# Kernel tuning notes

Hardware: AMD Instinct MI355X
Metric: run time of the kernel (lower is better)

The kernel has to match this reference:

```python
import jax, jax.numpy as jnp
import numpy as np

EPS = 1e-8

def _penalty(v, lo, hi):
    # if v<lo: (lo-v)/lo ; elif v>hi (hi finite): (v-hi)/hi ; else 0
    below = (lo - v) / lo
    if np.isinf(hi):
        return jnp.where(v < lo, below, 0.0)
    above = (v - hi) / hi
    return jnp.where(v < lo, below, jnp.where(v > hi, above, 0.0))

def _symbolic_features(x):
    # x: [B, input_dim]; column mapping from the original per-row loop
    am, bod, do, ph, nit = x[:, 0], x[:, 1], x[:, 2], x[:, 4], x[:, 7]
    # penalties in param_order = [ph, ammonia, bod, dissolved_oxygen, nitrate]
    p_ph  = _penalty(ph, 6.5, 8.5)
    p_am  = _penalty(am, 0.001, 0.5)
    p_bod = _penalty(bod, 0.001, 5.0)
    p_do  = _penalty(do, 6.0, np.inf)
    p_nit = _penalty(nit, 0.001, 10.0)
    # pollutant scores (missing params like 'nitrogen'/'orthophosphate' are skipped -> count adjusts)
    s_bact = (1.2 * am / (0.5 + EPS) + 1.5 * bod / (5.0 + EPS) - 0.8 * do / (10.0 + EPS)) / 3.0
    s_chem = (1.5 * ph / (8.5 + EPS) + 1.0 * nit / (10.0 + EPS)) / 2.0
    s_org  = (2.0 * bod / (5.0 + EPS) - 1.5 * do / (10.0 + EPS) + 0.8 * am / (0.5 + EPS)) / 3.0
    s_agr  = (2.0 * nit / (10.0 + EPS)) / 1.0
    resil = 1.0 / (1.0 + (p_ph + p_am + p_bod + p_do + p_nit) + EPS)
    return jnp.stack([p_ph, p_am, p_bod, p_do, p_nit, s_bact, s_chem, s_org, s_agr, resil], axis=1)

def setup_inputs() -> dict:
    key = jax.random.key(0)
    ks = jax.random.split(key, 16)
    B, D_IN, SYM, H = 1048576, 10, 10, 64
    def lin(k, fin, fout):
        k1, k2 = jax.random.split(k)
        s = 1.0 / np.sqrt(fin)
        return (jax.random.uniform(k1, (fin, fout), jnp.float32, -s, s),
                jax.random.uniform(k2, (fout,), jnp.float32, -s, s))
    W_sym, b_sym = lin(ks[0], SYM, H // 2)
    W_in, b_in = lin(ks[1], D_IN + H // 2, H)
    W1, b1 = lin(ks[2], H, H)
    W2, b2 = lin(ks[3], H, H)
    W3, b3 = lin(ks[4], H, H)
    W_r1, b_r1 = lin(ks[5], H, H // 2)
    W_r2, b_r2 = lin(ks[6], H // 2, 1)
    W_c1, b_c1 = lin(ks[7], H, H // 2)
    W_c2, b_c2 = lin(ks[8], H // 2, 4)
    x = jax.random.uniform(ks[9], (B, D_IN), jnp.float32)
    return {"x": x, "W_sym": W_sym, "b_sym": b_sym, "W_in": W_in, "b_in": b_in,
            "W1": W1, "b1": b1, "W2": W2, "b2": b2, "W3": W3, "b3": b3,
            "W_r1": W_r1, "b_r1": b_r1, "W_r2": W_r2, "b_r2": b_r2,
            "W_c1": W_c1, "b_c1": b_c1, "W_c2": W_c2, "b_c2": b_c2}

def reference(x, W_sym, b_sym, W_in, b_in, W1, b1, W2, b2, W3, b3,
              W_r1, b_r1, W_r2, b_r2, W_c1, b_c1, W_c2, b_c2):
    elu = jax.nn.elu
    sym = _symbolic_features(x)                      # [B, 10]
    sym_enc = elu(sym @ W_sym + b_sym)               # [B, 32]  (Dropout: eval mode = identity)
    h = elu(jnp.concatenate([x, sym_enc], axis=1) @ W_in + b_in)  # [B, 64]
    for W, b in ((W1, b1), (W2, b2), (W3, b3)):
        h = h + elu(h @ W + b)                       # residual MLP stack
    predictions = elu(h @ W_r1 + b_r1) @ W_r2 + b_r2            # [B, 1]
    pollutant_logits = elu(h @ W_c1 + b_c1) @ W_c2 + b_c2       # [B, 4]
    return predictions, pollutant_logits
```

## Files before the change

kernel.cpp:

```cpp
#include <hip/hip_runtime.h>
#include <hip/hip_bf16.h>
#include <math.h>

#define NROWS 1048576
#define EPSF 1e-8f
#define GRID 512
#define TPB 256
#define ITERS 16

typedef unsigned short ushortT;
typedef __attribute__((ext_vector_type(8))) short short8;
typedef __attribute__((ext_vector_type(4))) short short4v;
typedef __attribute__((ext_vector_type(4))) float floatx4;
typedef __attribute__((ext_vector_type(2))) int int2v;

#define WS_HI   256
#define WS_LO   41216
#define WS_MF   82176
#define MF_B5   0
#define MF_WSYM 320
#define MF_BSYM 640
#define MF_WR2  672
#define MF_BR2  704
#define MF_WC2  708
#define MF_BC2  836
#define MF_WC2T 840
#define MF_TOTAL 968

#define LDS_FENCE() asm volatile("s_waitcnt lgkmcnt(0)" ::: "memory")

struct WPtrs { const void* p[19]; };

__global__ void sniff_kernel(const ushortT* __restrict__ x, int* __restrict__ flag) {
    if (threadIdx.x == 0 && blockIdx.x == 0) {
        unsigned s = 0;
        for (int i = 0; i < 64; ++i) s |= (unsigned)(x[i] & 0x8000u);
        *flag = s ? 1 : 0;
    }
}

__device__ __forceinline__ float ldw(const void* p, int i, bool f32) {
    return f32 ? ((const float*)p)[i]
               : __uint_as_float(((unsigned)((const ushortT*)p)[i]) << 16);
}

__global__ void prep_kernel(WPtrs wp, const int* __restrict__ flag, void* __restrict__ ws) {
    const bool f32 = (*flag != 0);
    ushortT* hi = (ushortT*)((char*)ws + WS_HI);
    ushortT* lo = (ushortT*)((char*)ws + WS_LO);
    float* mf = (float*)((char*)ws + WS_MF);
    const int B = blockIdx.x;
    if (B < 5) {
        const int L = B;
        for (int idx = threadIdx.x; idx < 4096; idx += 256) {
            const int j8 = idx & 7, ln = (idx >> 3) & 63, s2 = (idx >> 9) & 1, t = idx >> 10;
            const int s = 2 * s2 + (j8 >> 2), j = j8 & 3;
            const int k = 16 * s + 4 * (ln >> 4) + j;
            const int m = 16 * t + (ln & 15);
            float w = 0.0f;
            if (L == 0)      { if (k < 42) w = ldw(wp.p[3], k * 64 + m, f32); }
            else if (L <= 3) { if (k < 64) w = ldw(wp.p[3 + 2 * L], k * 64 + m, f32); }
            else             { if (k < 64) w = (m < 32) ? ldw(wp.p[11], k * 32 + m, f32)
                                                        : ldw(wp.p[15], k * 32 + (m - 32), f32); }
            const unsigned u = __float_as_uint(w);
            const float rem = w - __uint_as_float(u & 0xffff0000u);
            hi[L * 4096 + idx] = (ushortT)(u >> 16);
            lo[L * 4096 + idx] = (ushortT)(__float_as_uint(rem) >> 16);
        }
    } else {
        const int src[12] = {4, 6, 8, 10, 12, 16, 1, 2, 13, 14, 17, 18};
        const int cnt[12] = {64, 64, 64, 64, 32, 32, 320, 32, 32, 1, 128, 4};
        const int dst[12] = {0, 64, 128, 192, 256, 288, MF_WSYM, MF_BSYM, MF_WR2, MF_BR2, MF_WC2, MF_BC2};
        for (int a = 0; a < 12; ++a)
            for (int i = threadIdx.x; i < cnt[a]; i += 256)
                mf[dst[a] + i] = ldw(wp.p[src[a]], i, f32);
        for (int i = threadIdx.x; i < 128; i += 256) {
            const int qq = i >> 5, j = i & 31;
            mf[MF_WC2T + i] = ldw(wp.p[17], j * 4 + qq, f32);
        }
    }
}

__device__ __forceinline__ float eluf(float v) {
    return fmaxf(v, 0.0f) + (__expf(fminf(v, 0.0f)) - 1.0f);
}

__device__ __forceinline__ unsigned pack_hi16(unsigned ua, unsigned ub) {
    return __builtin_amdgcn_perm(ub, ua, 0x07060302u);
}

__device__ __forceinline__ void split4(float a0, float a1, float a2, float a3,
                                       short4v& h4, short4v& l4) {
    const unsigned u0 = __float_as_uint(a0), u1 = __float_as_uint(a1);
    const unsigned u2 = __float_as_uint(a2), u3 = __float_as_uint(a3);
    int2v h, l;
    h[0] = (int)pack_hi16(u0, u1);
    h[1] = (int)pack_hi16(u2, u3);
    const float l0 = a0 - __uint_as_float(u0 & 0xffff0000u);
    const float l1 = a1 - __uint_as_float(u1 & 0xffff0000u);
    const float l2 = a2 - __uint_as_float(u2 & 0xffff0000u);
    const float l3 = a3 - __uint_as_float(u3 & 0xffff0000u);
    l[0] = (int)pack_hi16(__float_as_uint(l0), __float_as_uint(l1));
    l[1] = (int)pack_hi16(__float_as_uint(l2), __float_as_uint(l3));
    h4 = __builtin_bit_cast(short4v, h);
    l4 = __builtin_bit_cast(short4v, l);
}

__device__ __forceinline__ floatx4 mfma16(short4v a, short4v b, floatx4 c) {
#if __has_builtin(__builtin_amdgcn_mfma_f32_16x16x16bf16_1k)
    return __builtin_amdgcn_mfma_f32_16x16x16bf16_1k(a, b, c, 0, 0, 0);
#else
    floatx4 d;
    asm("v_mfma_f32_16x16x16_bf16 %0, %1, %2, %3" : "=v"(d) : "v"(a), "v"(b), "v"(c));
    return d;
#endif
}

template<bool F32>
__device__ __forceinline__ void run_body(
    const void* __restrict__ xin, const char* __restrict__ wsb,
    void* __restrict__ out,
    const ushortT* __restrict__ wlds,
    const float* __restrict__ mflds,
    float (* __restrict__ hb)[68],
    const int lane, const int wavebase)
{
    const ushortT* __restrict__ wflo = (const ushortT*)(wsb + WS_LO);
    const int n = lane & 15, q = lane >> 4;

    #pragma unroll
    for (int i = 0; i < 6; ++i) {
        const int c = 42 + q * 6 + i;
        if (c < 64) hb[n][c] = 0.0f;
    }

    unsigned xu[2][5];
    float xf[2][10];
    #pragma unroll
    for (int u = 0; u < 2; ++u) {
        const int rowg = wavebase + 16 * u + n;
        if (F32) {
            const float* xp = (const float*)xin + (size_t)rowg * 10;
            #pragma unroll
            for (int i = 0; i < 10; ++i) xf[u][i] = xp[i];
        } else {
            const unsigned* xd = (const unsigned*)((const ushortT*)xin + (size_t)rowg * 10);
            #pragma unroll
            for (int i = 0; i < 5; ++i) xu[u][i] = xd[i];
        }
    }

    #pragma unroll 1
    for (int it = 0; it < ITERS; ++it) {
        const int rowbase = wavebase + it * 32;
        short4v Bhi[2][4], Blo[2][4];

        #pragma unroll
        for (int u = 0; u < 2; ++u) {
            float x[10];
            if (F32) {
                #pragma unroll
                for (int i = 0; i < 10; ++i) x[i] = xf[u][i];
            } else {
                #pragma unroll
                for (int i = 0; i < 5; ++i) {
                    const unsigned d = xu[u][i];
                    x[2 * i]     = __uint_as_float(d << 16);
                    x[2 * i + 1] = __uint_as_float(d & 0xffff0000u);
                }
            }
            if (q == 0) {
                #pragma unroll
                for (int i = 0; i < 10; ++i) hb[n][i] = x[i];
            }

            const float am = x[0], bod = x[1], dox = x[2], ph = x[4], nit = x[7];
            const float p_ph  = ph  < 6.5f   ? (6.5f - ph) * 0.15384616f
                              : (ph > 8.5f   ? (ph - 8.5f) * 0.11764706f : 0.0f);
            const float p_am  = am  < 0.001f ? (0.001f - am) * 1000.0f
                              : (am > 0.5f   ? (am - 0.5f) * 2.0f : 0.0f);
            const float p_bod = bod < 0.001f ? (0.001f - bod) * 1000.0f
                              : (bod > 5.0f  ? (bod - 5.0f) * 0.2f : 0.0f);
            const float p_do  = dox < 6.0f   ? (6.0f - dox) * 0.16666667f : 0.0f;
            const float p_nit = nit < 0.001f ? (0.001f - nit) * 1000.0f
                              : (nit > 10.0f ? (nit - 10.0f) * 0.1f : 0.0f);
            const float s_bact = (am * 2.3999999f + bod * 0.29999998f - dox * 0.08f) * 0.33333334f;
            const float s_chem = (ph * 0.17647059f + nit * 0.1f) * 0.5f;
            const float s_org  = (bod * 0.39999998f - dox * 0.14999999f + am * 1.5999999f) * 0.33333334f;
            const float s_agr  = nit * 0.2f;
            const float resil  = 1.0f / (1.0f + (p_ph + p_am + p_bod + p_do + p_nit) + EPSF);
            const float sym[10] = {p_ph, p_am, p_bod, p_do, p_nit, s_bact, s_chem, s_org, s_agr, resil};

            float se[8];
            {
                const floatx4 b0 = *(const floatx4*)(mflds + MF_BSYM + q * 8);
                const floatx4 b1 = *(const floatx4*)(mflds + MF_BSYM + q * 8 + 4);
                #pragma unroll
                for (int jj = 0; jj < 4; ++jj) { se[jj] = b0[jj]; se[4 + jj] = b1[jj]; }
                #pragma unroll
                for (int k = 0; k < 10; ++k) {
                    const floatx4 w0 = *(const floatx4*)(mflds + MF_WSYM + k * 32 + q * 8);
                    const floatx4 w1 = *(const floatx4*)(mflds + MF_WSYM + k * 32 + q * 8 + 4);
                    #pragma unroll
                    for (int jj = 0; jj < 4; ++jj) {
                        se[jj]     = fmaf(sym[k], w0[jj], se[jj]);
                        se[4 + jj] = fmaf(sym[k], w1[jj], se[4 + jj]);
                    }
                }
            }
            #pragma unroll
            for (int jj = 0; jj < 8; ++jj) hb[n][10 + q * 8 + jj] = eluf(se[jj]);
            LDS_FENCE();
            #pragma unroll
            for (int s = 0; s < 4; ++s) {
                const floatx4 v = *(const floatx4*)&hb[n][16 * s + 4 * q];
                split4(v[0], v[1], v[2], v[3], Bhi[u][s], Blo[u][s]);
            }
            LDS_FENCE();
        }

        {
            const int itn = (it + 1 < ITERS) ? it + 1 : it;
            #pragma unroll
            for (int u = 0; u < 2; ++u) {
                const int rowg = wavebase + itn * 32 + 16 * u + n;
                if (F32) {
                    const float* xp = (const float*)xin + (size_t)rowg * 10;
                    #pragma unroll
                    for (int i = 0; i < 10; ++i) xf[u][i] = xp[i];
                } else {
                    const unsigned* xd = (const unsigned*)((const ushortT*)xin + (size_t)rowg * 10);
                    #pragma unroll
                    for (int i = 0; i < 5; ++i) xu[u][i] = xd[i];
                }
            }
        }

        float hprev[2][4][4];
        #pragma unroll
        for (int L = 0; L < 5; ++L) {
            short8 Ap[8];
            const ushortT* wl = wlds + L * 4096 + lane * 8;
            #pragma unroll
            for (int c = 0; c < 8; ++c)
                Ap[c] = *(const short8*)(wl + c * 512);
            short8 Alp[8];
            if (F32) {
                const int base = L * 4096 + lane * 8;
                #pragma unroll
                for (int c = 0; c < 8; ++c)
                    Alp[c] = *(const short8*)(wflo + base + c * 512);
            }

            floatx4 acc[2][4];
            #pragma unroll
            for (int t = 0; t < 4; ++t) {
                const floatx4 b = *(const floatx4*)(mflds + MF_B5 + L * 64 + 16 * t + 4 * q);
                acc[0][t] = b; acc[1][t] = b;
            }
            #pragma unroll
            for (int t = 0; t < 4; ++t) {
                #pragma unroll
                for (int s2 = 0; s2 < 2; ++s2) {
                    const short8 A = Ap[t * 2 + s2];
                    const short4v ae = {A[0], A[1], A[2], A[3]};
                    const short4v ao = {A[4], A[5], A[6], A[7]};
                    #pragma unroll
                    for (int u = 0; u < 2; ++u) {
                        acc[u][t] = mfma16(ae, Bhi[u][2 * s2],     acc[u][t]);
                        acc[u][t] = mfma16(ae, Blo[u][2 * s2],     acc[u][t]);
                        acc[u][t] = mfma16(ao, Bhi[u][2 * s2 + 1], acc[u][t]);
                        acc[u][t] = mfma16(ao, Blo[u][2 * s2 + 1], acc[u][t]);
                    }
                    if (F32) {
                        const short8 Al = Alp[t * 2 + s2];
                        const short4v le  = {Al[0], Al[1], Al[2], Al[3]};
                        const short4v lo_ = {Al[4], Al[5], Al[6], Al[7]};
                        #pragma unroll
                        for (int u = 0; u < 2; ++u) {
                            acc[u][t] = mfma16(le,  Bhi[u][2 * s2],     acc[u][t]);
                            acc[u][t] = mfma16(lo_, Bhi[u][2 * s2 + 1], acc[u][t]);
                        }
                    }
                }
            }

            if (L < 4) {
                #pragma unroll
                for (int u = 0; u < 2; ++u) {
                    #pragma unroll
                    for (int t = 0; t < 4; ++t) {
                        #pragma unroll
                        for (int r = 0; r < 4; ++r) {
                            float e = eluf(acc[u][t][r]);
                            if (L >= 1) e += hprev[u][t][r];
                            hprev[u][t][r] = e;
                        }
                        split4(hprev[u][t][0], hprev[u][t][1],
                               hprev[u][t][2], hprev[u][t][3], Bhi[u][t], Blo[u][t]);
                    }
                }
            } else {
                const floatx4 wr0 = *(const floatx4*)(mflds + MF_WR2 + 4 * q);
                const floatx4 wr1 = *(const floatx4*)(mflds + MF_WR2 + 16 + 4 * q);
                #pragma unroll
                for (int u = 0; u < 2; ++u) {
                    float pred = (q == 0) ? mflds[MF_BR2] : 0.0f;
                    float z2[4], z3[4];
                    #pragma unroll
                    for (int r = 0; r < 4; ++r) {
                        pred = fmaf(eluf(acc[u][0][r]), wr0[r], pred);
                        pred = fmaf(eluf(acc[u][1][r]), wr1[r], pred);
                        z2[r] = eluf(acc[u][2][r]);
                        z3[r] = eluf(acc[u][3][r]);
                    }
                    float lg[4];
                    #pragma unroll
                    for (int c = 0; c < 4; ++c) {
                        const floatx4 wc0 = *(const floatx4*)(mflds + MF_WC2T + c * 32 + 4 * q);
                        const floatx4 wc1 = *(const floatx4*)(mflds + MF_WC2T + c * 32 + 16 + 4 * q);
                        float l = (q == 0) ? mflds[MF_BC2 + c] : 0.0f;
                        #pragma unroll
                        for (int r = 0; r < 4; ++r) {
                            l = fmaf(z2[r], wc0[r], l);
                            l = fmaf(z3[r], wc1[r], l);
                        }
                        lg[c] = l;
                    }
                    pred += __shfl_xor(pred, 16, 64);
                    pred += __shfl_xor(pred, 32, 64);
                    #pragma unroll
                    for (int c = 0; c < 4; ++c) {
                        lg[c] += __shfl_xor(lg[c], 16, 64);
                        lg[c] += __shfl_xor(lg[c], 32, 64);
                    }
                    const float lsel = q == 0 ? lg[0] : (q == 1 ? lg[1] : (q == 2 ? lg[2] : lg[3]));
                    const int rowg = rowbase + 16 * u + n;
                    if (F32) {
                        float* o = (float*)out;
                        if (q == 0) o[rowg] = pred;
                        o[NROWS + rowg * 4 + q] = lsel;
                    } else {
                        __hip_bfloat16* o = (__hip_bfloat16*)out;
                        if (q == 0) o[rowg] = __float2bfloat16(pred);
                        o[NROWS + rowg * 4 + q] = __float2bfloat16(lsel);
                    }
                }
            }
        }
    }
}

__global__ __launch_bounds__(TPB, 2) void mlp_mfma_kernel(
    const void* __restrict__ xin, const int* __restrict__ flagp,
    const void* __restrict__ ws, void* __restrict__ out)
{
    __shared__ __align__(16) ushortT wlds[5 * 4096];
    __shared__ __align__(16) float mflds[MF_TOTAL];
    __shared__ float hball[4][16][68];

    const int tid = threadIdx.x;
    {
        const unsigned* src = (const unsigned*)((const char*)ws + WS_HI);
        unsigned* dst = (unsigned*)wlds;
        for (int i = tid; i < 10240; i += TPB) dst[i] = src[i];
        const float* mfsrc = (const float*)((const char*)ws + WS_MF);
        for (int i = tid; i < MF_TOTAL; i += TPB) mflds[i] = mfsrc[i];
    }
    __syncthreads();

    const int wave = tid >> 6, lane = tid & 63;
    const int gw = blockIdx.x * 4 + wave;
    const int wavebase = gw * (32 * ITERS);
    if (*flagp != 0)
        run_body<true>(xin, (const char*)ws, out, wlds, mflds, hball[wave], lane, wavebase);
    else
        run_body<false>(xin, (const char*)ws, out, wlds, mflds, hball[wave], lane, wavebase);
}

extern "C" void kernel_launch(void* const* d_in, const int* in_sizes, int n_in,
                              void* d_out, int out_size, void* d_ws, size_t ws_size,
                              hipStream_t stream) {
    (void)in_sizes; (void)n_in; (void)out_size; (void)ws_size;
    int* flag = (int*)d_ws;

    sniff_kernel<<<1, 64, 0, stream>>>((const ushortT*)d_in[0], flag);

    WPtrs wp;
    for (int i = 0; i < 19; ++i) wp.p[i] = d_in[i];
    prep_kernel<<<6, 256, 0, stream>>>(wp, flag, d_ws);

    mlp_mfma_kernel<<<GRID, TPB, 0, stream>>>(d_in[0], flag, d_ws, d_out);
}
```

Before: 330.6 us.

## Use 16x16x32 bf16 MFMA, stream weights from global, drop sniff launch, raise occupancy

Replaces pairs of 16x16x16 bf16 MFMAs with single 16x16x32 MFMAs by packing B operands into short8. Removes the LDS copy of the weight matrices so each lane reads its A fragments straight from the workspace through cache. This frees about 40KB of LDS, which allows launch bounds of 4 blocks per SM, and the grid is doubled while iterations per wave are halved. The separate sniff kernel is dropped in favour of a ballot-based dtype check inside each kernel. The cost is more global/L2 traffic for weights on every layer, in exchange for fewer MFMA issues, one less launch, and higher occupancy.

```diff
diff --git a/kernel.cpp b/kernel.cpp
--- a/kernel.cpp
+++ b/kernel.cpp
@@ -4,9 +4,9 @@
 
 #define NROWS 1048576
 #define EPSF 1e-8f
-#define GRID 512
+#define GRID 1024
 #define TPB 256
-#define ITERS 16
+#define ITERS 8
 
 typedef unsigned short ushortT;
 typedef __attribute__((ext_vector_type(8))) short short8;
@@ -31,21 +31,26 @@
 
 struct WPtrs { const void* p[19]; };
 
-__global__ void sniff_kernel(const ushortT* __restrict__ x, int* __restrict__ flag) {
-    if (threadIdx.x == 0 && blockIdx.x == 0) {
-        unsigned s = 0;
-        for (int i = 0; i < 64; ++i) s |= (unsigned)(x[i] & 0x8000u);
-        *flag = s ? 1 : 0;
-    }
-}
-
 __device__ __forceinline__ float ldw(const void* p, int i, bool f32) {
     return f32 ? ((const float*)p)[i]
                : __uint_as_float(((unsigned)((const ushortT*)p)[i]) << 16);
 }
 
-__global__ void prep_kernel(WPtrs wp, const int* __restrict__ flag, void* __restrict__ ws) {
-    const bool f32 = (*flag != 0);
+__device__ __forceinline__ int sniff_f32(const void* x) {
+    const ushortT v = ((const ushortT*)x)[threadIdx.x & 63];
+    const unsigned long long m = __ballot((v & 0x8000u) != 0);
+    return (m != 0ull) ? 1 : 0;
+}
+
+__global__ void prep_kernel(WPtrs wp, void* __restrict__ ws) {
+    __shared__ int flagS;
+    if (threadIdx.x < 64) {
+        const int f = sniff_f32(wp.p[0]);
+        if (threadIdx.x == 0) flagS = f;
+    }
+    __syncthreads();
+    const bool f32 = (flagS != 0);
+
     ushortT* hi = (ushortT*)((char*)ws + WS_HI);
     ushortT* lo = (ushortT*)((char*)ws + WS_LO);
     float* mf = (float*)((char*)ws + WS_MF);
@@ -106,13 +111,20 @@
     l4 = __builtin_bit_cast(short4v, l);
 }
 
-__device__ __forceinline__ floatx4 mfma16(short4v a, short4v b, floatx4 c) {
-#if __has_builtin(__builtin_amdgcn_mfma_f32_16x16x16bf16_1k)
-    return __builtin_amdgcn_mfma_f32_16x16x16bf16_1k(a, b, c, 0, 0, 0);
+__device__ __forceinline__ void put4(short8& d, int hh, short4v s) {
+    d[4 * hh + 0] = s[0]; d[4 * hh + 1] = s[1];
+    d[4 * hh + 2] = s[2]; d[4 * hh + 3] = s[3];
+}
+
+__device__ __forceinline__ floatx4 mfma32(short8 a, short8 b, floatx4 c) {
+#if __has_builtin(__builtin_amdgcn_mfma_f32_16x16x32_bf16)
+    return __builtin_amdgcn_mfma_f32_16x16x32_bf16(a, b, c, 0, 0, 0);
 #else
-    floatx4 d;
-    asm("v_mfma_f32_16x16x16_bf16 %0, %1, %2, %3" : "=v"(d) : "v"(a), "v"(b), "v"(c));
-    return d;
+    const short4v ae = {a[0], a[1], a[2], a[3]}, ao = {a[4], a[5], a[6], a[7]};
+    const short4v be = {b[0], b[1], b[2], b[3]}, bo = {b[4], b[5], b[6], b[7]};
+    c = __builtin_amdgcn_mfma_f32_16x16x16bf16_1k(ae, be, c, 0, 0, 0);
+    c = __builtin_amdgcn_mfma_f32_16x16x16bf16_1k(ao, bo, c, 0, 0, 0);
+    return c;
 #endif
 }
 
@@ -120,12 +132,12 @@
 __device__ __forceinline__ void run_body(
     const void* __restrict__ xin, const char* __restrict__ wsb,
     void* __restrict__ out,
-    const ushortT* __restrict__ wlds,
     const float* __restrict__ mflds,
     float (* __restrict__ hb)[68],
     const int lane, const int wavebase)
 {
-    const ushortT* __restrict__ wflo = (const ushortT*)(wsb + WS_LO);
+    const short8* __restrict__ Ahi = (const short8*)(wsb + WS_HI) + lane;
+    const short8* __restrict__ Alo = (const short8*)(wsb + WS_LO) + lane;
     const int n = lane & 15, q = lane >> 4;
 
     #pragma unroll
@@ -153,7 +165,7 @@
     #pragma unroll 1
     for (int it = 0; it < ITERS; ++it) {
         const int rowbase = wavebase + it * 32;
-        short4v Bhi[2][4], Blo[2][4];
+        short8 Bhi8[2][2], Blo8[2][2];
 
         #pragma unroll
         for (int u = 0; u < 2; ++u) {
@@ -212,9 +224,15 @@
             for (int jj = 0; jj < 8; ++jj) hb[n][10 + q * 8 + jj] = eluf(se[jj]);
             LDS_FENCE();
             #pragma unroll
-            for (int s = 0; s < 4; ++s) {
-                const floatx4 v = *(const floatx4*)&hb[n][16 * s + 4 * q];
-                split4(v[0], v[1], v[2], v[3], Bhi[u][s], Blo[u][s]);
+            for (int s2 = 0; s2 < 2; ++s2) {
+                #pragma unroll
+                for (int hh = 0; hh < 2; ++hh) {
+                    const floatx4 v = *(const floatx4*)&hb[n][16 * (2 * s2 + hh) + 4 * q];
+                    short4v h4, l4;
+                    split4(v[0], v[1], v[2], v[3], h4, l4);
+                    put4(Bhi8[u][s2], hh, h4);
+                    put4(Blo8[u][s2], hh, l4);
+                }
             }
             LDS_FENCE();
         }
@@ -240,16 +258,12 @@
         #pragma unroll
         for (int L = 0; L < 5; ++L) {
             short8 Ap[8];
-            const ushortT* wl = wlds + L * 4096 + lane * 8;
-            #pragma unroll
-            for (int c = 0; c < 8; ++c)
-                Ap[c] = *(const short8*)(wl + c * 512);
+            #pragma unroll
+            for (int c = 0; c < 8; ++c) Ap[c] = Ahi[L * 512 + c * 64];
             short8 Alp[8];
             if (F32) {
-                const int base = L * 4096 + lane * 8;
-                #pragma unroll
-                for (int c = 0; c < 8; ++c)
-                    Alp[c] = *(const short8*)(wflo + base + c * 512);
+                #pragma unroll
+                for (int c = 0; c < 8; ++c) Alp[c] = Alo[L * 512 + c * 64];
             }
 
             floatx4 acc[2][4];
@@ -262,25 +276,17 @@
             for (int t = 0; t < 4; ++t) {
                 #pragma unroll
                 for (int s2 = 0; s2 < 2; ++s2) {
-                    const short8 A = Ap[t * 2 + s2];
-                    const short4v ae = {A[0], A[1], A[2], A[3]};
-                    const short4v ao = {A[4], A[5], A[6], A[7]};
+                    const short8 A = Ap[2 * t + s2];
                     #pragma unroll
                     for (int u = 0; u < 2; ++u) {
-                        acc[u][t] = mfma16(ae, Bhi[u][2 * s2],     acc[u][t]);
-                        acc[u][t] = mfma16(ae, Blo[u][2 * s2],     acc[u][t]);
-                        acc[u][t] = mfma16(ao, Bhi[u][2 * s2 + 1], acc[u][t]);
-                        acc[u][t] = mfma16(ao, Blo[u][2 * s2 + 1], acc[u][t]);
+                        acc[u][t] = mfma32(A, Bhi8[u][s2], acc[u][t]);
+                        acc[u][t] = mfma32(A, Blo8[u][s2], acc[u][t]);
                     }
                     if (F32) {
-                        const short8 Al = Alp[t * 2 + s2];
-                        const short4v le  = {Al[0], Al[1], Al[2], Al[3]};
-                        const short4v lo_ = {Al[4], Al[5], Al[6], Al[7]};
+                        const short8 Al = Alp[2 * t + s2];
                         #pragma unroll
-                        for (int u = 0; u < 2; ++u) {
-                            acc[u][t] = mfma16(le,  Bhi[u][2 * s2],     acc[u][t]);
-                            acc[u][t] = mfma16(lo_, Bhi[u][2 * s2 + 1], acc[u][t]);
-                        }
+                        for (int u = 0; u < 2; ++u)
+                            acc[u][t] = mfma32(Al, Bhi8[u][s2], acc[u][t]);
                     }
                 }
             }
@@ -296,8 +302,11 @@
                             if (L >= 1) e += hprev[u][t][r];
                             hprev[u][t][r] = e;
                         }
+                        short4v h4, l4;
                         split4(hprev[u][t][0], hprev[u][t][1],
-                               hprev[u][t][2], hprev[u][t][3], Bhi[u][t], Blo[u][t]);
+                               hprev[u][t][2], hprev[u][t][3], h4, l4);
+                        put4(Bhi8[u][t >> 1], t & 1, h4);
+                        put4(Blo8[u][t >> 1], t & 1, l4);
                     }
                 }
             } else {
@@ -351,19 +360,19 @@
     }
 }
 
-__global__ __launch_bounds__(TPB, 2) void mlp_mfma_kernel(
-    const void* __restrict__ xin, const int* __restrict__ flagp,
-    const void* __restrict__ ws, void* __restrict__ out)
+__global__ __launch_bounds__(TPB, 4) void mlp_mfma_kernel(
+    const void* __restrict__ xin, const void* __restrict__ ws, void* __restrict__ out)
 {
-    __shared__ __align__(16) ushortT wlds[5 * 4096];
     __shared__ __align__(16) float mflds[MF_TOTAL];
     __shared__ float hball[4][16][68];
+    __shared__ int flagS;
 
     const int tid = threadIdx.x;
+    if (tid < 64) {
+        const int f = sniff_f32(xin);
+        if (tid == 0) flagS = f;
+    }
     {
-        const unsigned* src = (const unsigned*)((const char*)ws + WS_HI);
-        unsigned* dst = (unsigned*)wlds;
-        for (int i = tid; i < 10240; i += TPB) dst[i] = src[i];
         const float* mfsrc = (const float*)((const char*)ws + WS_MF);
         for (int i = tid; i < MF_TOTAL; i += TPB) mflds[i] = mfsrc[i];
     }
@@ -372,23 +381,20 @@
     const int wave = tid >> 6, lane = tid & 63;
     const int gw = blockIdx.x * 4 + wave;
     const int wavebase = gw * (32 * ITERS);
-    if (*flagp != 0)
-        run_body<true>(xin, (const char*)ws, out, wlds, mflds, hball[wave], lane, wavebase);
+    if (flagS != 0)
+        run_body<true>(xin, (const char*)ws, out, mflds, hball[wave], lane, wavebase);
     else
-        run_body<false>(xin, (const char*)ws, out, wlds, mflds, hball[wave], lane, wavebase);
+        run_body<false>(xin, (const char*)ws, out, mflds, hball[wave], lane, wavebase);
 }
 
 extern "C" void kernel_launch(void* const* d_in, const int* in_sizes, int n_in,
                               void* d_out, int out_size, void* d_ws, size_t ws_size,
                               hipStream_t stream) {
     (void)in_sizes; (void)n_in; (void)out_size; (void)ws_size;
-    int* flag = (int*)d_ws;
-
-    sniff_kernel<<<1, 64, 0, stream>>>((const ushortT*)d_in[0], flag);
 
     WPtrs wp;
     for (int i = 0; i < 19; ++i) wp.p[i] = d_in[i];
-    prep_kernel<<<6, 256, 0, stream>>>(wp, flag, d_ws);
-
-    mlp_mfma_kernel<<<GRID, TPB, 0, stream>>>(d_in[0], flag, d_ws, d_out);
-}
+    prep_kernel<<<6, 256, 0, stream>>>(wp, d_ws);
+
+    mlp_mfma_kernel<<<GRID, TPB, 0, stream>>>(d_in[0], d_ws, d_out);
+}
```

Measured after the change: 522.8 us. 1.58x slower.
